# Kernel tuning notes

Hardware: AMD Instinct MI355X
Metric: run time of the kernel (lower is better)

The kernel has to match this reference:

```python
import jax, jax.numpy as jnp
import numpy as np
import math

NPAD = 100      # npadding
NLAYERS = 4     # transformer_num_layers
NHEAD = 8       # transformer_nhead


def _posenc(T, d):
    pos = jnp.arange(T, dtype=jnp.float32)[:, None]
    div = jnp.exp(jnp.arange(0, d, 2, dtype=jnp.float32) * (-(math.log(1000.0) / d)))
    pe = jnp.zeros((T, d), jnp.float32)
    pe = pe.at[:, 0::2].set(jnp.sin(pos * div))
    pe = pe.at[:, 1::2].set(jnp.cos(pos * div))
    return pe


def _ln(x, g, b):
    m = x.mean(-1, keepdims=True)
    v = ((x - m) ** 2).mean(-1, keepdims=True)
    return (x - m) / jnp.sqrt(v + 1e-5) * g + b


def conv_individual(Y, kernel, npadding):
    # Y: (B,N,Ttot); kernel: (ntau,N). Causal zero-pad then FFT conv (faithful to source).
    B, N, Ttot = Y.shape
    kernel = jnp.concatenate([jnp.zeros((1, N), kernel.dtype), kernel], axis=0)
    ntau = kernel.shape[0]
    nn = Ttot + ntau - 1
    Yf = jnp.fft.fft(Y, n=nn, axis=2)                 # (B,N,nn) complex
    Kf = jnp.fft.fft(kernel.T, n=nn, axis=-1)          # (N,nn)
    c = jnp.fft.ifft(Yf * Kf[None], axis=2).real
    c = jnp.where(jnp.abs(c) < 1e-5, 0.0, c)           # ad-hoc small-value zeroing from source
    return c[:, :, :Ttot][:, :, npadding:]             # (B,N,T)


def conv_subspace(Y, kernel, npadding):
    # Y: (B,N,Ttot); kernel: (ntau,S) -> G: (B,N,S,T)
    B, N, Ttot = Y.shape
    k = kernel[None]                                   # (1,ntau,S)
    k = jnp.concatenate([jnp.zeros((1, 1, k.shape[2]), jnp.float32), k], axis=1)
    ntau = k.shape[1]
    nn = Ttot + ntau - 1
    Yf = jnp.fft.fft(Y, n=nn, axis=2)[..., None]       # (B,N,nn,1)
    Kf = jnp.fft.fft(k, n=nn, axis=1)[None]            # (1,1,nn,S)
    G = jnp.fft.ifft(Yf * Kf, axis=2).real             # (B,N,nn,S)
    G = jnp.where(jnp.abs(G) < 1e-5, 0.0, G)
    G = G[:, :, :Ttot, :][:, :, npadding:, :]
    return jnp.swapaxes(G, -1, -2)                     # (B,N,S,T)


def _encoder(x, Wqkv, bqkv, Wo, bo, ln1_g, ln1_b, W1, b1, W2, b2, ln2_g, ln2_b):
    B, T, D = x.shape
    hd = D // NHEAD
    for l in range(NLAYERS):
        qkv = x @ Wqkv[l] + bqkv[l]                    # (B,T,3D)
        q, k, v = jnp.split(qkv, 3, axis=-1)
        q = q.reshape(B, T, NHEAD, hd)
        k = k.reshape(B, T, NHEAD, hd)
        v = v.reshape(B, T, NHEAD, hd)
        scores = jnp.einsum('bthd,bshd->bhts', q, k) / jnp.sqrt(jnp.float32(hd))
        attn = jax.nn.softmax(scores, axis=-1)
        o = jnp.einsum('bhts,bshd->bthd', attn, v).reshape(B, T, D)
        x = _ln(x + (o @ Wo[l] + bo[l]), ln1_g[l], ln1_b[l])
        ff = jax.nn.gelu(x @ W1[l] + b1[l], approximate=False) @ W2[l] + b2[l]
        x = _ln(x + ff, ln2_g[l], ln2_b[l])
    return x


def reference(Y, token_W, token_b, Wqkv, bqkv, Wo, bo, ln1_g, ln1_b, W1, b1, W2, b2,
              ln2_g, ln2_b, toL_W, toL_b, dec_W1, dec_b1, dec_W2, dec_b2,
              stimulus_basis, readout_W, coupling_W, coupling_basis, self_kernel):
    B, N, Ttot = Y.shape
    T = Ttot - NPAD
    D = token_W.shape[1]
    # token conversion over time (seq dim = time)
    x = jnp.swapaxes(Y[:, :, NPAD:], 1, 2) @ token_W + token_b   # (B,T,D)
    x = x + _posenc(T, D)[None]
    x = _encoder(x, Wqkv, bqkv, Wo, bo, ln1_g, ln1_b, W1, b1, W2, b2, ln2_g, ln2_b)
    pooled = x.mean(axis=1)                                      # (B,D)
    h = pooled @ toL_W + toL_b                                   # (B,2Z)
    Z = h.shape[1] // 2
    z = h[:, :Z]                                                 # mu (sample_latent=False)
    # stimulus decoder (2-layer MLP)
    coeffs = jax.nn.relu(z @ dec_W1 + dec_b1) @ dec_W2 + dec_b2  # (B, NF*NB)
    NB = stimulus_basis.shape[1]
    NF = coeffs.shape[1] // NB
    coeffs = coeffs.reshape(B, NF, NB)
    sti_lat = jnp.einsum('bfk,tk->bft', coeffs, stimulus_basis)  # (B,NF,T)
    sti = jnp.einsum('nf,bft->bnt', readout_W, sti_lat)          # (B,N,T)
    # coupling via FFT causal conv into subspaces
    G = conv_subspace(Y, coupling_basis, NPAD)                   # (B,N,S,T)
    cpl = jnp.einsum('ns,bnst->bnt', coupling_W, G)
    # self-history FFT causal conv
    slf = conv_individual(Y, self_kernel, NPAD)
    return sti + cpl + slf                                       # log firing rate (B,N,T)


def setup_inputs() -> dict:
    key = jax.random.key(0)
    ks = jax.random.split(key, 30)
    B, N, Ttot = 16, 256, 1100
    D, FF, Zdim = 256, 1024, 64
    NB, NF, S, NTAU = 30, 4, 4, 20   # NF = narea*stimulus_nfactor = 2*2
    T = Ttot - NPAD
    sc = 0.02
    inp = {
        'Y': jax.random.uniform(ks[0], (B, N, Ttot), jnp.float32),
        'token_W': jax.random.normal(ks[1], (N, D), jnp.float32) * sc,
        'token_b': jnp.zeros((D,), jnp.float32),
        'Wqkv': jax.random.normal(ks[2], (NLAYERS, D, 3 * D), jnp.float32) * sc,
        'bqkv': jnp.zeros((NLAYERS, 3 * D), jnp.float32),
        'Wo': jax.random.normal(ks[3], (NLAYERS, D, D), jnp.float32) * sc,
        'bo': jnp.zeros((NLAYERS, D), jnp.float32),
        'ln1_g': jnp.ones((NLAYERS, D), jnp.float32),
        'ln1_b': jnp.zeros((NLAYERS, D), jnp.float32),
        'W1': jax.random.normal(ks[4], (NLAYERS, D, FF), jnp.float32) * sc,
        'b1': jnp.zeros((NLAYERS, FF), jnp.float32),
        'W2': jax.random.normal(ks[5], (NLAYERS, FF, D), jnp.float32) * sc,
        'b2': jnp.zeros((NLAYERS, D), jnp.float32),
        'ln2_g': jnp.ones((NLAYERS, D), jnp.float32),
        'ln2_b': jnp.zeros((NLAYERS, D), jnp.float32),
        'toL_W': jax.random.normal(ks[6], (D, 2 * Zdim), jnp.float32) * sc,
        'toL_b': jnp.zeros((2 * Zdim,), jnp.float32),
        'dec_W1': jax.random.normal(ks[7], (Zdim, 2 * Zdim), jnp.float32) * sc,
        'dec_b1': jnp.zeros((2 * Zdim,), jnp.float32),
        'dec_W2': jax.random.normal(ks[8], (2 * Zdim, NB * NF), jnp.float32) * sc * 0.001,
        'dec_b2': jnp.zeros((NB * NF,), jnp.float32),
        'stimulus_basis': jax.random.normal(ks[9], (T, NB), jnp.float32),
        'readout_W': jax.random.normal(ks[10], (N, NF), jnp.float32) * sc,
        'coupling_W': jax.random.normal(ks[11], (N, S), jnp.float32) * sc,
        'coupling_basis': jax.random.normal(ks[12], (NTAU, S), jnp.float32) * 0.1,
        'self_kernel': jax.random.normal(ks[13], (NTAU, N), jnp.float32) * 0.1,
    }
    return inp
```

## Files before the change

kernel.cpp:

```cpp
#include <hip/hip_runtime.h>
#include <math.h>

#define TT_   1000
#define TTOT_ 1100
#define NPAD_ 100
#define DD_   256
#define NN_   256

#define X_OFF    0u
#define XB_OFF   4096000u
#define O_OFF    6144000u
#define BIG_OFF  12288000u
#define WT_OFF   20480000u
#define PE_OFF   22085632u
#define PP_OFF   22341632u
#define PL_OFF   (PP_OFF + 32768u)
#define CF_OFF   (PL_OFF + 4096u)
#define CB_OFF   (CF_OFF + 1920u)
#define BQ_OFF   (CB_OFF + 5120u)
#define STL_OFF  (BQ_OFF + 3072u)

#define SC2_ 0.25503902254649546f

typedef __attribute__((ext_vector_type(8))) short s16x8;
typedef __attribute__((ext_vector_type(4))) float f32x4;
typedef __attribute__((ext_vector_type(16))) float f32x16;
typedef __attribute__((ext_vector_type(4))) unsigned u32x4;

__device__ inline short f2bf(float f) {
    unsigned u = __float_as_uint(f);
    u += 0x7fffu + ((u >> 16) & 1u);
    return (short)(u >> 16);
}
__device__ inline float exp2i(float x) {
    float r; asm("v_exp_f32 %0, %1" : "=v"(r) : "v"(x)); return r;
}

__device__ inline void gl_lds16(const short* g, short* l) {
    __builtin_amdgcn_global_load_lds(
        (const __attribute__((address_space(1))) void*)g,
        (__attribute__((address_space(3))) void*)l, 16, 0, 0);
}

__global__ __launch_bounds__(256) void wtr_k(const float* __restrict__ in,
                                             short* __restrict__ out, int K, int N,
                                             int qrows, float qs)
{
    __shared__ float t[32][33];
    const int n0 = blockIdx.x * 32, k0 = blockIdx.y * 32;
    in  += (size_t)blockIdx.z * K * N;
    out += (size_t)blockIdx.z * K * N;
    const int tx = threadIdx.x & 31, ty = threadIdx.x >> 5;
    #pragma unroll
    for (int i = 0; i < 4; ++i)
        t[ty + 8 * i][tx] = in[(size_t)(k0 + ty + 8 * i) * N + n0 + tx];
    __syncthreads();
    #pragma unroll
    for (int i = 0; i < 4; ++i) {
        const int row = n0 + ty + 8 * i;
        float f = t[tx][ty + 8 * i];
        if (row < qrows) f *= qs;
        out[(size_t)row * K + k0 + tx] = f2bf(f);
    }
}

__global__ __launch_bounds__(256) void ytr_k(const float* __restrict__ Y,
                                             short* __restrict__ out)
{
    __shared__ float t[32][33];
    const int b = blockIdx.z;
    const int t0 = blockIdx.x * 32, n0 = blockIdx.y * 32;
    const int tx = threadIdx.x & 31, ty = threadIdx.x >> 5;
    #pragma unroll
    for (int i = 0; i < 4; ++i) {
        const int tt = t0 + tx;
        t[ty + 8 * i][tx] = (tt < TT_)
            ? Y[((size_t)(b * NN_ + n0 + ty + 8 * i)) * TTOT_ + NPAD_ + tt] : 0.f;
    }
    __syncthreads();
    #pragma unroll
    for (int i = 0; i < 4; ++i) {
        const int tt = t0 + ty + 8 * i;
        if (tt < TT_)
            out[((size_t)(b * TT_ + tt)) * NN_ + n0 + tx] = f2bf(t[tx][ty + 8 * i]);
    }
}

__global__ void pe_k(float* __restrict__ PE)
{
    const int t = blockIdx.x, d = threadIdx.x;
    const float div = __expf(-(float)(d & ~1) * 0.0269834190585241f);
    const float ang = (float)t * div;
    PE[t * 256 + d] = (d & 1) ? cosf(ang) : sinf(ang);
}

__global__ void bscale_k(const float* __restrict__ in, float* __restrict__ out)
{
    const int i = blockIdx.x * 256 + threadIdx.x;
    if (i < 3072) {
        const int col = i % 768;
        out[i] = in[i] * ((col < 256) ? SC2_ : 1.f);
    }
}

template<int OUTBF, int ACT, int RES, int DUAL>
__global__ __launch_bounds__(256) void bgemm_k(const short* __restrict__ A,
                                               const short* __restrict__ Bt,
                                               const float* __restrict__ bias,
                                               const float* __restrict__ resid,
                                               void* __restrict__ Cout,
                                               short* __restrict__ Cb,
                                               int M, int N, int K, int nby)
{
    __shared__ short As[64 * 64];
    __shared__ short Bs[128 * 64];
    const int tid = threadIdx.x;

    const int nwg = gridDim.x;
    int gid = blockIdx.x;
    {
        const int q = nwg >> 3, r = nwg & 7;
        const int x = gid & 7, idx = gid >> 3;
        gid = (x < r ? x * (q + 1) : r * (q + 1) + (x - r) * q) + idx;
    }
    const int bx = gid / nby, by = gid - bx * nby;
    const int m0 = bx * 64, n0 = by * 128;

    const int wv = tid >> 6, lane = tid & 63;
    const int wr = wv >> 1, wc = wv & 1;
    const int l15 = lane & 15, lg = lane >> 4;

    f32x4 acc[2][4];
    #pragma unroll
    for (int i = 0; i < 2; ++i)
        #pragma unroll
        for (int j = 0; j < 4; ++j) acc[i][j] = (f32x4){0.f, 0.f, 0.f, 0.f};

    const int nt = K >> 6;
    for (int t = 0; t < nt; ++t) {
        __syncthreads();
        const int k0 = t << 6;
        #pragma unroll
        for (int i = 0; i < 2; ++i) {
            const int cid = i * 256 + tid;
            const int r = cid >> 3, c = cid & 7;
            gl_lds16(A + (size_t)(m0 + r) * K + k0 + ((c ^ (r & 7)) * 8), As + cid * 8);
        }
        #pragma unroll
        for (int i = 0; i < 4; ++i) {
            const int cid = i * 256 + tid;
            const int r = cid >> 3, c = cid & 7;
            gl_lds16(Bt + (size_t)(n0 + r) * K + k0 + ((c ^ (r & 7)) * 8), Bs + cid * 8);
        }
        __syncthreads();

        #pragma unroll
        for (int ks = 0; ks < 2; ++ks) {
            s16x8 af[2], bf[4];
            #pragma unroll
            for (int mi = 0; mi < 2; ++mi) {
                const int row = wr * 32 + mi * 16 + l15;
                const int ch = ks * 4 + lg;
                af[mi] = *(const s16x8*)(As + row * 64 + ((ch ^ (row & 7)) * 8));
            }
            #pragma unroll
            for (int ni = 0; ni < 4; ++ni) {
                const int col = wc * 64 + ni * 16 + l15;
                const int ch = ks * 4 + lg;
                bf[ni] = *(const s16x8*)(Bs + col * 64 + ((ch ^ (col & 7)) * 8));
            }
            #pragma unroll
            for (int mi = 0; mi < 2; ++mi)
                #pragma unroll
                for (int ni = 0; ni < 4; ++ni)
                    acc[mi][ni] = __builtin_amdgcn_mfma_f32_16x16x32_bf16(
                        af[mi], bf[ni], acc[mi][ni], 0, 0, 0);
        }
    }

    #pragma unroll
    for (int mi = 0; mi < 2; ++mi) {
        #pragma unroll
        for (int ni = 0; ni < 4; ++ni) {
            const int col = n0 + wc * 64 + ni * 16 + l15;
            const float bv = bias[col];
            #pragma unroll
            for (int r = 0; r < 4; ++r) {
                const int row = m0 + wr * 32 + mi * 16 + lg * 4 + r;
                float v = acc[mi][ni][r] + bv;
                if (RES == 1) v += resid[(size_t)row * N + col];
                if (RES == 2) v += resid[(size_t)(row % 1000) * N + col];
                if (ACT) v = 0.5f * v * (1.0f + erff(v * 0.70710678118654752f));
                if (OUTBF) ((short*)Cout)[(size_t)row * N + col] = f2bf(v);
                else       ((float*)Cout)[(size_t)row * N + col] = v;
                if (DUAL)  Cb[(size_t)row * N + col] = f2bf(v);
            }
        }
    }
}

__global__ __launch_bounds__(512) void bgemmln_k(const short* __restrict__ A,
                                                 const short* __restrict__ Bt,
                                                 const float* __restrict__ bias,
                                                 const float* __restrict__ lng,
                                                 const float* __restrict__ lnb,
                                                 float* __restrict__ X,
                                                 short* __restrict__ Xb,
                                                 int K)
{
    __shared__ short As[64 * 64];
    __shared__ short Bs[256 * 64];
    __shared__ float red[64][4][2];
    __shared__ float mrs[64][2];
    const int tid = threadIdx.x;

    const int nwg = gridDim.x;
    int gid = blockIdx.x;
    {
        const int q = nwg >> 3, r = nwg & 7;
        const int x = gid & 7, idx = gid >> 3;
        gid = (x < r ? x * (q + 1) : r * (q + 1) + (x - r) * q) + idx;
    }
    const int m0 = gid * 64;

    const int wv = tid >> 6, lane = tid & 63;
    const int wr = wv >> 2, wcx = wv & 3;
    const int l15 = lane & 15, lg = lane >> 4;

    f32x4 acc[2][4];
    #pragma unroll
    for (int i = 0; i < 2; ++i)
        #pragma unroll
        for (int j = 0; j < 4; ++j) acc[i][j] = (f32x4){0.f, 0.f, 0.f, 0.f};

    const int nt = K >> 6;
    for (int t = 0; t < nt; ++t) {
        __syncthreads();
        const int k0 = t << 6;
        {
            const int r = tid >> 3, c = tid & 7;
            gl_lds16(A + (size_t)(m0 + r) * K + k0 + ((c ^ (r & 7)) * 8), As + tid * 8);
        }
        #pragma unroll
        for (int i = 0; i < 4; ++i) {
            const int cid = i * 512 + tid;
            const int r = cid >> 3, c = cid & 7;
            gl_lds16(Bt + (size_t)r * K + k0 + ((c ^ (r & 7)) * 8), Bs + cid * 8);
        }
        __syncthreads();

        #pragma unroll
        for (int ks = 0; ks < 2; ++ks) {
            s16x8 af[2], bf[4];
            #pragma unroll
            for (int mi = 0; mi < 2; ++mi) {
                const int row = wr * 32 + mi * 16 + l15;
                const int ch = ks * 4 + lg;
                af[mi] = *(const s16x8*)(As + row * 64 + ((ch ^ (row & 7)) * 8));
            }
            #pragma unroll
            for (int ni = 0; ni < 4; ++ni) {
                const int col = wcx * 64 + ni * 16 + l15;
                const int ch = ks * 4 + lg;
                bf[ni] = *(const s16x8*)(Bs + col * 64 + ((ch ^ (col & 7)) * 8));
            }
            #pragma unroll
            for (int mi = 0; mi < 2; ++mi)
                #pragma unroll
                for (int ni = 0; ni < 4; ++ni)
                    acc[mi][ni] = __builtin_amdgcn_mfma_f32_16x16x32_bf16(
                        af[mi], bf[ni], acc[mi][ni], 0, 0, 0);
        }
    }

    float v[2][4][4];
    #pragma unroll
    for (int mi = 0; mi < 2; ++mi)
        #pragma unroll
        for (int ni = 0; ni < 4; ++ni) {
            const int col = wcx * 64 + ni * 16 + l15;
            const float bv = bias[col];
            #pragma unroll
            for (int r = 0; r < 4; ++r) {
                const int row = m0 + wr * 32 + mi * 16 + lg * 4 + r;
                v[mi][ni][r] = acc[mi][ni][r] + bv + X[(size_t)row * 256 + col];
            }
        }

    #pragma unroll
    for (int mi = 0; mi < 2; ++mi)
        #pragma unroll
        for (int r = 0; r < 4; ++r) {
            float ss = v[mi][0][r] + v[mi][1][r] + v[mi][2][r] + v[mi][3][r];
            float qq = v[mi][0][r] * v[mi][0][r] + v[mi][1][r] * v[mi][1][r]
                     + v[mi][2][r] * v[mi][2][r] + v[mi][3][r] * v[mi][3][r];
            #pragma unroll
            for (int msk = 1; msk < 16; msk <<= 1) {
                ss += __shfl_xor(ss, msk);
                qq += __shfl_xor(qq, msk);
            }
            if (l15 == 0) {
                const int rloc = wr * 32 + mi * 16 + lg * 4 + r;
                red[rloc][wcx][0] = ss;
                red[rloc][wcx][1] = qq;
            }
        }
    __syncthreads();
    if (tid < 64) {
        const float s = red[tid][0][0] + red[tid][1][0] + red[tid][2][0] + red[tid][3][0];
        const float q = red[tid][0][1] + red[tid][1][1] + red[tid][2][1] + red[tid][3][1];
        const float mean = s * (1.f / 256.f);
        const float var = q * (1.f / 256.f) - mean * mean;
        mrs[tid][0] = mean;
        mrs[tid][1] = rsqrtf(var + 1e-5f);
    }
    __syncthreads();

    #pragma unroll
    for (int mi = 0; mi < 2; ++mi)
        #pragma unroll
        for (int ni = 0; ni < 4; ++ni) {
            const int col = wcx * 64 + ni * 16 + l15;
            const float gg = lng[col], bb = lnb[col];
            #pragma unroll
            for (int r = 0; r < 4; ++r) {
                const int rloc = wr * 32 + mi * 16 + lg * 4 + r;
                const int row = m0 + rloc;
                const float o = (v[mi][ni][r] - mrs[rloc][0]) * mrs[rloc][1] * gg + bb;
                X[(size_t)row * 256 + col] = o;
                Xb[(size_t)row * 256 + col] = f2bf(o);
            }
        }
}

__global__ __launch_bounds__(256) void mattn_k(const short* __restrict__ qkv,
                                               short* __restrict__ o)
{
    int wg = blockIdx.x;
    wg = (wg & 7) * 128 + (wg >> 3);
    const int qt = wg & 7, h = (wg >> 3) & 7, b = wg >> 6;

    const int tid = threadIdx.x, wv = tid >> 6, lane = tid & 63;
    const int q31 = lane & 31, hi = lane >> 5;
    __shared__ short Ks[2][64 * 40];
    __shared__ short VT[2][32 * 72];

    const int q0w = qt * 128 + wv * 32;
    int qrow = q0w + q31; if (qrow > 999) qrow = 999;
    s16x8 bq[2];
    #pragma unroll
    for (int dh = 0; dh < 2; ++dh)
        bq[dh] = *(const s16x8*)(qkv + ((size_t)(b * TT_ + qrow)) * 768 + h * 32 + dh * 16 + hi * 8);

    f32x16 oacc;
    #pragma unroll
    for (int i = 0; i < 16; ++i) oacc[i] = 0.f;
    float lrun = 0.f;

    const int sr = tid >> 2, sc = tid & 3;
    const int kp = tid >> 3, dq = (tid & 7) * 4;
    s16x8 kreg;
    short4 va, vb;
    auto LOADT = [&](int kt) {
        int t = kt * 64 + sr; if (t > 999) t = 999;
        kreg = *(const s16x8*)(qkv + ((size_t)(b * TT_ + t)) * 768 + 256 + h * 32 + sc * 8);
        int t0 = kt * 64 + 2 * kp, t1 = t0 + 1;
        if (t0 > 999) t0 = 999;
        if (t1 > 999) t1 = 999;
        va = *(const short4*)(qkv + ((size_t)(b * TT_ + t0)) * 768 + 512 + h * 32 + dq);
        vb = *(const short4*)(qkv + ((size_t)(b * TT_ + t1)) * 768 + 512 + h * 32 + dq);
    };
    auto WRITET = [&](int buf) {
        *(s16x8*)(&Ks[buf][sr * 40 + sc * 8]) = kreg;
        const int c = kp >> 2;
        const int ko = (2 * kp) & 7;
        #pragma unroll
        for (int j = 0; j < 4; ++j) {
            const int d = dq + j;
            const unsigned pk = ((unsigned)(unsigned short)((&va.x)[j]))
                              | (((unsigned)(unsigned short)((&vb.x)[j])) << 16);
            *(unsigned*)(&VT[buf][d * 72 + ((c ^ (d >> 3)) * 8) + ko]) = pk;
        }
    };

    LOADT(0); WRITET(0);
    __syncthreads();
    int cur = 0;

    for (int kt = 0; kt < 16; ++kt) {
        if (kt < 15) LOADT(kt + 1);

        f32x16 st[2];
        __builtin_amdgcn_s_setprio(1);
        #pragma unroll
        for (int kb = 0; kb < 2; ++kb) {
            s16x8 kf0 = *(const s16x8*)(&Ks[cur][(kb * 32 + q31) * 40 + hi * 8]);
            s16x8 kf1 = *(const s16x8*)(&Ks[cur][(kb * 32 + q31) * 40 + 16 + hi * 8]);
            f32x16 z;
            #pragma unroll
            for (int i = 0; i < 16; ++i) z[i] = 0.f;
            z = __builtin_amdgcn_mfma_f32_32x32x16_bf16(kf0, bq[0], z, 0, 0, 0);
            z = __builtin_amdgcn_mfma_f32_32x32x16_bf16(kf1, bq[1], z, 0, 0, 0);
            st[kb] = z;
        }
        __builtin_amdgcn_s_setprio(0);

        if (kt == 15) {
            #pragma unroll
            for (int kb = 0; kb < 2; ++kb)
                #pragma unroll
                for (int r = 0; r < 16; ++r) {
                    const int kloc = kb * 32 + (r & 3) + 8 * (r >> 2) + 4 * hi;
                    if (960 + kloc >= TT_) st[kb][r] = -1e30f;
                }
        }

        float sloc = 0.f;
        #pragma unroll
        for (int kb = 0; kb < 2; ++kb)
            #pragma unroll
            for (int r = 0; r < 16; ++r) {
                const float p = exp2i(st[kb][r]);
                st[kb][r] = p; sloc += p;
            }
        lrun += sloc;

        unsigned wk[2][4][2];
        #pragma unroll
        for (int kb = 0; kb < 2; ++kb)
            #pragma unroll
            for (int a = 0; a < 4; ++a)
                #pragma unroll
                for (int h2 = 0; h2 < 2; ++h2) {
                    unsigned rr;
                    asm("v_cvt_pk_bf16_f32 %0, %1, %2"
                        : "=v"(rr)
                        : "v"(st[kb][4 * a + 2 * h2]), "v"(st[kb][4 * a + 2 * h2 + 1]));
                    wk[kb][a][h2] = rr;
                }

        #pragma unroll
        for (int ks = 0; ks < 4; ++ks) {
            const int kb = ks >> 1, qq = ks & 1;
            unsigned W[4];
            #pragma unroll
            for (int h2 = 0; h2 < 2; ++h2) {
                const unsigned send = hi ? wk[kb][2 * qq][h2] : wk[kb][2 * qq + 1][h2];
                const unsigned recv = __shfl_xor(send, 32);
                W[h2]     = hi ? recv : wk[kb][2 * qq][h2];
                W[2 + h2] = hi ? wk[kb][2 * qq + 1][h2] : recv;
            }
            u32x4 w4 = (u32x4){W[0], W[1], W[2], W[3]};
            s16x8 pb = __builtin_bit_cast(s16x8, w4);
            s16x8 vf = *(const s16x8*)(&VT[cur][q31 * 72 + (((2 * ks + hi) ^ (q31 >> 3)) * 8)]);
            __builtin_amdgcn_s_setprio(1);
            oacc = __builtin_amdgcn_mfma_f32_32x32x16_bf16(vf, pb, oacc, 0, 0, 0);
            __builtin_amdgcn_s_setprio(0);
        }

        if (kt < 15) WRITET(cur ^ 1);
        __syncthreads();
        cur ^= 1;
    }

    lrun += __shfl_xor(lrun, 32);

    const int t = q0w + q31;
    if (t < TT_) {
        const float inv = 1.f / lrun;
        short* ob = o + ((size_t)(b * TT_ + t)) * 256 + h * 32;
        #pragma unroll
        for (int a = 0; a < 4; ++a) {
            unsigned w0, w1;
            asm("v_cvt_pk_bf16_f32 %0, %1, %2"
                : "=v"(w0) : "v"(oacc[4 * a + 0] * inv), "v"(oacc[4 * a + 1] * inv));
            asm("v_cvt_pk_bf16_f32 %0, %1, %2"
                : "=v"(w1) : "v"(oacc[4 * a + 2] * inv), "v"(oacc[4 * a + 3] * inv));
            const int d0 = 8 * a + 4 * hi;
            *(unsigned*)(ob + d0) = w0;
            *(unsigned*)(ob + d0 + 2) = w1;
        }
    }
}

__global__ __launch_bounds__(256) void pool_part_k(const float* __restrict__ X,
                                                   float* __restrict__ partial)
{
    const int b = blockIdx.x, seg = blockIdx.y, d = threadIdx.x;
    float s = 0.f;
    const int t0 = seg * 125;
    for (int t = t0; t < t0 + 125; ++t) s += X[((size_t)b * TT_ + t) * 256 + d];
    partial[(b * 8 + seg) * 256 + d] = s;
}
__global__ __launch_bounds__(256) void pool_red_k(const float* __restrict__ partial,
                                                  float* __restrict__ pooled)
{
    const int b = blockIdx.x, d = threadIdx.x;
    float s = 0.f;
    for (int k = 0; k < 8; ++k) s += partial[(b * 8 + k) * 256 + d];
    pooled[b * 256 + d] = s * (1.f / (float)TT_);
}

__global__ __launch_bounds__(128) void head_k(const float* __restrict__ pooled,
                                              const float* __restrict__ toLW,
                                              const float* __restrict__ toLb,
                                              const float* __restrict__ dW1,
                                              const float* __restrict__ db1,
                                              const float* __restrict__ dW2,
                                              const float* __restrict__ db2,
                                              float* __restrict__ coeffs)
{
    const int b = blockIdx.x, j = threadIdx.x;
    __shared__ float hs[64];
    __shared__ float hid[128];
    float a = toLb[j];
    for (int d = 0; d < 256; ++d) a += pooled[b * 256 + d] * toLW[d * 128 + j];
    if (j < 64) hs[j] = a;
    __syncthreads();
    float a2 = db1[j];
    for (int z = 0; z < 64; ++z) a2 += hs[z] * dW1[z * 128 + j];
    hid[j] = fmaxf(a2, 0.f);
    __syncthreads();
    if (j < 120) {
        float a3 = db2[j];
        for (int k = 0; k < 128; ++k) a3 += hid[k] * dW2[k * 120 + j];
        coeffs[b * 120 + j] = a3;
    }
}

__global__ void comb_k(const float* __restrict__ selfK,
                       const float* __restrict__ cplW,
                       const float* __restrict__ cplB,
                       float* __restrict__ comb)
{
    const int n = threadIdx.x;
    for (int ti = 0; ti < 20; ++ti) {
        float s = selfK[ti * 256 + n];
        #pragma unroll
        for (int si = 0; si < 4; ++si) s += cplW[n * 4 + si] * cplB[ti * 4 + si];
        comb[n * 20 + ti] = s;
    }
}

__global__ __launch_bounds__(256) void stilat_k(const float* __restrict__ SB,
                                                const float* __restrict__ coeffs,
                                                float* __restrict__ STL)
{
    const int bf = blockIdx.x;
    __shared__ float c[30];
    if (threadIdx.x < 30) c[threadIdx.x] = coeffs[(bf >> 2) * 120 + (bf & 3) * 30 + threadIdx.x];
    __syncthreads();
    for (int t = threadIdx.x; t < TT_; t += 256) {
        float acc = 0.f;
        const float* sp = SB + (size_t)t * 30;
        #pragma unroll
        for (int k = 0; k < 30; ++k) acc += c[k] * sp[k];
        STL[bf * TT_ + t] = acc;
    }
}

__global__ __launch_bounds__(256) void final_k(const float* __restrict__ Y,
                                               const float* __restrict__ STL,
                                               const float* __restrict__ roW,
                                               const float* __restrict__ comb,
                                               float* __restrict__ out)
{
    const int bx = blockIdx.x;
    const int ts = bx & 3, nc = (bx >> 2) & 31, b = bx >> 7;
    const int n0 = nc * 8, t0 = ts * 250;
    const int tid = threadIdx.x;
    __shared__ float rw[8][4], ck[8][20], yl[8][272];

    if (tid < 32) rw[tid >> 2][tid & 3] = roW[(n0 + (tid >> 2)) * 4 + (tid & 3)];
    if (tid >= 64 && tid < 224) {
        const int j = tid - 64;
        ck[j / 20][j % 20] = comb[(n0 + j / 20) * 20 + (j % 20)];
    }
    for (int j = tid; j < 2160; j += 256) {
        const int n = j / 270, jj = j - n * 270;
        yl[n][jj] = Y[((size_t)(b * 256 + n0 + n)) * TTOT_ + t0 + 80 + jj];
    }
    __syncthreads();

    if (tid < 250) {
        const int t = t0 + tid;
        float s4[4];
        #pragma unroll
        for (int f = 0; f < 4; ++f) s4[f] = STL[((size_t)b * 4 + f) * TT_ + t];
        #pragma unroll
        for (int n = 0; n < 8; ++n) {
            float acc = rw[n][0] * s4[0] + rw[n][1] * s4[1]
                      + rw[n][2] * s4[2] + rw[n][3] * s4[3];
            #pragma unroll
            for (int tau = 1; tau <= 20; ++tau)
                acc += ck[n][tau - 1] * yl[n][tid + 20 - tau];
            out[((size_t)(b * 256 + n0 + n)) * TT_ + t] = acc;
        }
    }
}

extern "C" void kernel_launch(void* const* d_in, const int* in_sizes, int n_in,
                              void* d_out, int out_size, void* d_ws, size_t ws_size,
                              hipStream_t stream)
{
    const float* Y      = (const float*)d_in[0];
    const float* tokW   = (const float*)d_in[1];
    const float* tokb   = (const float*)d_in[2];
    const float* Wqkv   = (const float*)d_in[3];
    const float* bqkv   = (const float*)d_in[4];
    const float* Wo     = (const float*)d_in[5];
    const float* bo     = (const float*)d_in[6];
    const float* ln1g   = (const float*)d_in[7];
    const float* ln1b   = (const float*)d_in[8];
    const float* W1     = (const float*)d_in[9];
    const float* b1     = (const float*)d_in[10];
    const float* W2     = (const float*)d_in[11];
    const float* b2     = (const float*)d_in[12];
    const float* ln2g   = (const float*)d_in[13];
    const float* ln2b   = (const float*)d_in[14];
    const float* toLW   = (const float*)d_in[15];
    const float* toLb   = (const float*)d_in[16];
    const float* dW1    = (const float*)d_in[17];
    const float* db1    = (const float*)d_in[18];
    const float* dW2    = (const float*)d_in[19];
    const float* db2    = (const float*)d_in[20];
    const float* SB     = (const float*)d_in[21];
    const float* roW    = (const float*)d_in[22];
    const float* cplW   = (const float*)d_in[23];
    const float* cplB   = (const float*)d_in[24];
    const float* selfK  = (const float*)d_in[25];

    float* ws  = (float*)d_ws;
    float* X   = ws + X_OFF;
    short* Xb  = (short*)(ws + XB_OFF);
    short* O   = (short*)(ws + O_OFF);
    short* BIG = (short*)(ws + BIG_OFF);
    short* WT  = (short*)(ws + WT_OFF);
    float* PE  = ws + PE_OFF;
    float* PP  = ws + PP_OFF;
    float* PL  = ws + PL_OFF;
    float* CF  = ws + CF_OFF;
    float* CB  = ws + CB_OFF;
    float* BQ  = ws + BQ_OFF;
    float* STL = ws + STL_OFF;

    short* WTqkv = WT;
    short* WTo   = WT + 786432;
    short* WTw1  = WT + 1048576;
    short* WTw2  = WT + 2097152;
    short* WTtok = WT + 3145728;
    short* Ybt   = BIG;

    wtr_k<<<dim3(24, 8, 4), 256, 0, stream>>>(Wqkv, WTqkv, 256, 768, 256, SC2_);
    wtr_k<<<dim3(8, 8, 4),  256, 0, stream>>>(Wo,   WTo,   256, 256, 0, 1.f);
    wtr_k<<<dim3(32, 8, 4), 256, 0, stream>>>(W1,   WTw1,  256, 1024, 0, 1.f);
    wtr_k<<<dim3(8, 32, 4), 256, 0, stream>>>(W2,   WTw2,  1024, 256, 0, 1.f);
    wtr_k<<<dim3(8, 8, 1),  256, 0, stream>>>(tokW, WTtok, 256, 256, 0, 1.f);
    bscale_k<<<12, 256, 0, stream>>>(bqkv, BQ);
    pe_k<<<1000, 256, 0, stream>>>(PE);
    ytr_k<<<dim3(32, 8, 16), 256, 0, stream>>>(Y, Ybt);

    bgemm_k<0, 0, 2, 1><<<500, 256, 0, stream>>>(
        Ybt, WTtok, tokb, PE, X, Xb, 16000, 256, 256, 2);

    for (int l = 0; l < 4; ++l) {
        bgemm_k<1, 0, 0, 0><<<1500, 256, 0, stream>>>(
            Xb, WTqkv + (size_t)l * 196608, BQ + l * 768, nullptr, BIG, nullptr,
            16000, 768, 256, 6);
        mattn_k<<<1024, 256, 0, stream>>>(BIG, O);
        bgemmln_k<<<250, 512, 0, stream>>>(
            O, WTo + (size_t)l * 65536, bo + l * 256,
            ln1g + l * 256, ln1b + l * 256, X, Xb, 256);
        bgemm_k<1, 1, 0, 0><<<2000, 256, 0, stream>>>(
            Xb, WTw1 + (size_t)l * 262144, b1 + l * 1024, nullptr, BIG, nullptr,
            16000, 1024, 256, 8);
        bgemmln_k<<<250, 512, 0, stream>>>(
            BIG, WTw2 + (size_t)l * 262144, b2 + l * 256,
            ln2g + l * 256, ln2b + l * 256, X, Xb, 1024);
    }

    pool_part_k<<<dim3(16, 8), 256, 0, stream>>>(X, PP);
    pool_red_k<<<16, 256, 0, stream>>>(PP, PL);
    head_k<<<16, 128, 0, stream>>>(PL, toLW, toLb, dW1, db1, dW2, db2, CF);
    comb_k<<<1, 256, 0, stream>>>(selfK, cplW, cplB, CB);
    stilat_k<<<64, 256, 0, stream>>>(SB, CF, STL);
    final_k<<<2048, 256, 0, stream>>>(Y, STL, roW, CB, (float*)d_out);
}
```

Baseline: 518.2 us.

## Use 512-thread attention blocks with split K/V loaders and permlane swaps

The attention kernel now runs 512 threads per block, covering 256 query rows instead of 128, so each shared-memory K/V tile is reused by twice as many waves. K and V tile loads are split across the two thread halves. The V transpose packing now uses byte-permute instructions, and the cross-half P exchange uses v_permlane32_swap instead of shuffles plus selects. It halves global K/V traffic per query, at the risk of lower occupancy and more padding waste on the last query tile (1000 rows into 4 tiles of 256).

```diff
diff --git a/kernel.cpp b/kernel.cpp
--- a/kernel.cpp
+++ b/kernel.cpp
@@ -333,19 +333,19 @@
         }
 }
 
-__global__ __launch_bounds__(256) void mattn_k(const short* __restrict__ qkv,
+__global__ __launch_bounds__(512) void mattn_k(const short* __restrict__ qkv,
                                                short* __restrict__ o)
 {
     int wg = blockIdx.x;
-    wg = (wg & 7) * 128 + (wg >> 3);
-    const int qt = wg & 7, h = (wg >> 3) & 7, b = wg >> 6;
+    wg = (wg & 7) * 64 + (wg >> 3);
+    const int qt = wg & 3, h = (wg >> 2) & 7, b = wg >> 5;
 
     const int tid = threadIdx.x, wv = tid >> 6, lane = tid & 63;
     const int q31 = lane & 31, hi = lane >> 5;
     __shared__ short Ks[2][64 * 40];
     __shared__ short VT[2][32 * 72];
 
-    const int q0w = qt * 128 + wv * 32;
+    const int q0w = qt * 256 + wv * 32;
     int qrow = q0w + q31; if (qrow > 999) qrow = 999;
     s16x8 bq[2];
     #pragma unroll
@@ -358,28 +358,40 @@
     float lrun = 0.f;
 
     const int sr = tid >> 2, sc = tid & 3;
-    const int kp = tid >> 3, dq = (tid & 7) * 4;
+    const int u = tid & 255;
+    const int kp = u >> 3, dq = (u & 7) * 4;
     s16x8 kreg;
     short4 va, vb;
     auto LOADT = [&](int kt) {
-        int t = kt * 64 + sr; if (t > 999) t = 999;
-        kreg = *(const s16x8*)(qkv + ((size_t)(b * TT_ + t)) * 768 + 256 + h * 32 + sc * 8);
-        int t0 = kt * 64 + 2 * kp, t1 = t0 + 1;
-        if (t0 > 999) t0 = 999;
-        if (t1 > 999) t1 = 999;
-        va = *(const short4*)(qkv + ((size_t)(b * TT_ + t0)) * 768 + 512 + h * 32 + dq);
-        vb = *(const short4*)(qkv + ((size_t)(b * TT_ + t1)) * 768 + 512 + h * 32 + dq);
+        if (tid < 256) {
+            int t = kt * 64 + sr; if (t > 999) t = 999;
+            kreg = *(const s16x8*)(qkv + ((size_t)(b * TT_ + t)) * 768 + 256 + h * 32 + sc * 8);
+        } else {
+            int t0 = kt * 64 + 2 * kp, t1 = t0 + 1;
+            if (t0 > 999) t0 = 999;
+            if (t1 > 999) t1 = 999;
+            va = *(const short4*)(qkv + ((size_t)(b * TT_ + t0)) * 768 + 512 + h * 32 + dq);
+            vb = *(const short4*)(qkv + ((size_t)(b * TT_ + t1)) * 768 + 512 + h * 32 + dq);
+        }
     };
     auto WRITET = [&](int buf) {
-        *(s16x8*)(&Ks[buf][sr * 40 + sc * 8]) = kreg;
-        const int c = kp >> 2;
-        const int ko = (2 * kp) & 7;
-        #pragma unroll
-        for (int j = 0; j < 4; ++j) {
-            const int d = dq + j;
-            const unsigned pk = ((unsigned)(unsigned short)((&va.x)[j]))
-                              | (((unsigned)(unsigned short)((&vb.x)[j])) << 16);
-            *(unsigned*)(&VT[buf][d * 72 + ((c ^ (d >> 3)) * 8) + ko]) = pk;
+        if (tid < 256) {
+            *(s16x8*)(&Ks[buf][sr * 40 + sc * 8]) = kreg;
+        } else {
+            const int c = kp >> 2;
+            const int ko = (2 * kp) & 7;
+            const uint2 vaw = *(const uint2*)&va;
+            const uint2 vbw = *(const uint2*)&vb;
+            unsigned pk[4];
+            pk[0] = __builtin_amdgcn_perm(vbw.x, vaw.x, 0x05040100u);
+            pk[1] = __builtin_amdgcn_perm(vbw.x, vaw.x, 0x07060302u);
+            pk[2] = __builtin_amdgcn_perm(vbw.y, vaw.y, 0x05040100u);
+            pk[3] = __builtin_amdgcn_perm(vbw.y, vaw.y, 0x07060302u);
+            #pragma unroll
+            for (int j = 0; j < 4; ++j) {
+                const int d = dq + j;
+                *(unsigned*)(&VT[buf][d * 72 + ((c ^ (d >> 3)) * 8) + ko]) = pk[j];
+            }
         }
     };
 
@@ -442,15 +454,11 @@
         #pragma unroll
         for (int ks = 0; ks < 4; ++ks) {
             const int kb = ks >> 1, qq = ks & 1;
-            unsigned W[4];
-            #pragma unroll
-            for (int h2 = 0; h2 < 2; ++h2) {
-                const unsigned send = hi ? wk[kb][2 * qq][h2] : wk[kb][2 * qq + 1][h2];
-                const unsigned recv = __shfl_xor(send, 32);
-                W[h2]     = hi ? recv : wk[kb][2 * qq][h2];
-                W[2 + h2] = hi ? wk[kb][2 * qq + 1][h2] : recv;
-            }
-            u32x4 w4 = (u32x4){W[0], W[1], W[2], W[3]};
+            unsigned X0 = wk[kb][2 * qq + 1][0], Y0 = wk[kb][2 * qq][0];
+            unsigned X1 = wk[kb][2 * qq + 1][1], Y1 = wk[kb][2 * qq][1];
+            asm("v_permlane32_swap_b32 %0, %1" : "+v"(X0), "+v"(Y0));
+            asm("v_permlane32_swap_b32 %0, %1" : "+v"(X1), "+v"(Y1));
+            u32x4 w4 = (u32x4){Y0, Y1, X0, X1};
             s16x8 pb = __builtin_bit_cast(s16x8, w4);
             s16x8 vf = *(const s16x8*)(&VT[cur][q31 * 72 + (((2 * ks + hi) ^ (q31 >> 3)) * 8)]);
             __builtin_amdgcn_s_setprio(1);
@@ -667,7 +675,7 @@
         bgemm_k<1, 0, 0, 0><<<1500, 256, 0, stream>>>(
             Xb, WTqkv + (size_t)l * 196608, BQ + l * 768, nullptr, BIG, nullptr,
             16000, 768, 256, 6);
-        mattn_k<<<1024, 256, 0, stream>>>(BIG, O);
+        mattn_k<<<512, 512, 0, stream>>>(BIG, O);
         bgemmln_k<<<250, 512, 0, stream>>>(
             O, WTo + (size_t)l * 65536, bo + l * 256,
             ln1g + l * 256, ln1b + l * 256, X, Xb, 256);
```

Measured after the change: 497.3 us. -4.0%, faster.
